# Kernel optimization log

Hardware: AMD Instinct MI355X
Metric: run time of the kernel (lower is better)

Reference implementation:

```python
import jax, jax.numpy as jnp
import numpy as np

B, T, C = 2, 2048, 2048
H, DK, DV, K = 16, 128, 128, 4
KEY_DIM = H * DK
VALUE_DIM = H * DV
CONV_DIM = 2 * KEY_DIM + VALUE_DIM
EPS = 1e-6


def setup_inputs() -> dict:
    key = jax.random.key(0)
    ks = jax.random.split(key, 6)
    s = 0.02
    return {
        "x": jax.random.normal(ks[0], (B, T, C), jnp.float32),
        "input_pos": jnp.arange(T, dtype=jnp.int32),
        "W_qkvz": jax.random.normal(ks[1], (C, CONV_DIM + VALUE_DIM), jnp.float32) * s,
        "W_b": jax.random.normal(ks[2], (C, H), jnp.float32) * s,
        "W_a": jax.random.normal(ks[3], (C, H), jnp.float32) * s,
        "conv_w": jax.random.normal(ks[4], (CONV_DIM, 1, K), jnp.float32) * 0.3,
        "norm_w": jnp.ones((DV,), jnp.float32),
        "W_out": jax.random.normal(ks[5], (VALUE_DIM, C), jnp.float32) * s,
        "conv_state": jnp.zeros((B, CONV_DIM, K), jnp.float32),
        "recurrent_state": jnp.zeros((B, H, DK, DV), jnp.float32),
    }


def _l2norm(a):
    return a / jnp.maximum(jnp.linalg.norm(a, axis=-1, keepdims=True), 1e-12)


def reference(x, input_pos, W_qkvz, W_b, W_a, conv_w, norm_w, W_out,
              conv_state, recurrent_state):
    Bx, Tx, Cx = x.shape
    # reset state when sequence starts at position 0
    keep = 1.0 - (input_pos[0] == 0).astype(x.dtype)
    conv_state = conv_state * keep
    recurrent_state = recurrent_state * keep

    qkvz = x @ W_qkvz                                  # [B,T,conv_dim+value_dim]
    qkv, z = qkvz[..., :CONV_DIM], qkvz[..., CONV_DIM:]
    z = z.reshape(Bx, Tx, H, DV)
    beta = jax.nn.sigmoid(x @ W_b)                     # [B,T,H]
    alpha = jax.nn.sigmoid(x @ W_a)                    # [B,T,H]

    # depthwise causal conv with carried conv_state prefix
    conv_in = jnp.concatenate([conv_state, qkv.transpose(0, 2, 1)], axis=-1)  # [B,conv_dim,K+T]
    y = jax.lax.conv_general_dilated(
        conv_in, conv_w, window_strides=(1,), padding='VALID',
        dimension_numbers=('NCH', 'OIH', 'NCH'), feature_group_count=CONV_DIM)
    y = jax.nn.silu(y[:, :, -Tx:]).transpose(0, 2, 1)  # [B,T,conv_dim]

    q, k, v = jnp.split(y, [KEY_DIM, 2 * KEY_DIM], axis=-1)
    q = _l2norm(q.reshape(Bx, Tx, H, DK))
    k = _l2norm(k.reshape(Bx, Tx, H, DK))
    v = v.reshape(Bx, Tx, H, DV)

    def step(state, xs):
        q_i, k_i, v_i, a_i, b_i = xs                    # [B,H,Dk],[B,H,Dk],[B,H,Dv],[B,H],[B,H]
        new_state = (a_i[..., None, None] * state
                     + b_i[..., None, None] * (k_i[..., :, None] * v_i[..., None, :]))
        out_i = jnp.einsum('bhk,bhkv->bhv', q_i, new_state)
        return new_state, out_i

    xs = (q.transpose(1, 0, 2, 3), k.transpose(1, 0, 2, 3), v.transpose(1, 0, 2, 3),
          alpha.transpose(1, 0, 2), beta.transpose(1, 0, 2))
    _, outs = jax.lax.scan(step, recurrent_state, xs)   # outs: [T,B,H,Dv]
    output = outs.transpose(1, 0, 2, 3)                 # [B,T,H,Dv]

    # RMSNorm over head_v_dim, then gate by sigmoid(z)
    output = output * jax.lax.rsqrt(jnp.mean(output * output, axis=-1, keepdims=True) + EPS) * norm_w
    output = output * jax.nn.sigmoid(z)
    return output.reshape(Bx, Tx, -1) @ W_out
```

## Files before the change

kernel.cpp:

```cpp
#include <hip/hip_runtime.h>
#include <hip/hip_bf16.h>
#include <math.h>

#define Bb 2
#define Tt 2048
#define Cc 2048
#define Hh 16
#define CONVD 6144
#define Mrows 4096
#define NCHUNK 32

typedef __attribute__((ext_vector_type(8))) short short8v;
typedef __attribute__((ext_vector_type(4))) float floatx4;

__device__ __forceinline__ unsigned short f2bf(float f) {
    __hip_bfloat16 h = __float2bfloat16(f);
    return __builtin_bit_cast(unsigned short, h);
}

__device__ __forceinline__ void load_lds16(const void* g, void* l) {
    __builtin_amdgcn_global_load_lds(
        (const __attribute__((address_space(1))) void*)g,
        (__attribute__((address_space(3))) void*)l, 16, 0, 0);
}

__device__ __forceinline__ int swz8(int col) {
    return col ^ (((col >> 5) & 3) << 3);
}

__global__ __launch_bounds__(256) void cast_bf16(
    const float* __restrict__ in, unsigned short* __restrict__ out, long n)
{
    long i = ((long)blockIdx.x * 256 + threadIdx.x) * 4;
    if (i + 3 >= n) return;
    float4 f = *(const float4*)(in + i);
    ushort4 o;
    o.x = f2bf(f.x); o.y = f2bf(f.y); o.z = f2bf(f.z); o.w = f2bf(f.w);
    *(ushort4*)(out + i) = o;
}

__global__ __launch_bounds__(256) void transpose_cast(
    const float* __restrict__ W, unsigned short* __restrict__ WT, int Kk, int Nn)
{
    __shared__ float tile[32][33];
    const int n0 = blockIdx.x * 32;
    const int k0 = blockIdx.y * 32;
    const int tx = threadIdx.x & 31;
    const int ty = threadIdx.x >> 5;
#pragma unroll
    for (int r = ty; r < 32; r += 8)
        tile[r][tx] = W[(size_t)(k0 + r) * Nn + n0 + tx];
    __syncthreads();
#pragma unroll
    for (int r = ty; r < 32; r += 8)
        WT[(size_t)(n0 + r) * Kk + k0 + tx] = f2bf(tile[tx][r]);
}

__global__ __launch_bounds__(256) void gemm_bf16(
    const unsigned short* __restrict__ A, const unsigned short* __restrict__ Bt,
    float* __restrict__ C, int Kk, int lda, int ldb, int ldc)
{
    __shared__ __align__(16) unsigned short A_lds[128 * 64];
    __shared__ __align__(16) unsigned short B_lds[128 * 64];

    const int tid = threadIdx.x;
    const int wv = tid >> 6;
    const int lane = tid & 63;
    const int wr = wv >> 1, wc = wv & 1;
    const int l15 = lane & 15, kq = lane >> 4;
    const int rsw = (l15 & 7) << 3;
    const int block_m = blockIdx.y * 128;
    const int block_n = blockIdx.x * 128;

    const int srow = lane >> 3;
    const int scol = ((lane & 7) ^ srow) << 3;

    floatx4 acc[4][4] = {};

    for (int k0 = 0; k0 < Kk; k0 += 64) {
#pragma unroll
        for (int i = 0; i < 4; ++i) {
            const int lq = wv * 4 + i;
            const unsigned short* asrc =
                A + (size_t)(block_m + lq * 8 + srow) * lda + k0 + scol;
            load_lds16(asrc, &A_lds[lq * 512]);
            const unsigned short* bsrc =
                Bt + (size_t)(block_n + lq * 8 + srow) * ldb + k0 + scol;
            load_lds16(bsrc, &B_lds[lq * 512]);
        }
        __syncthreads();

#pragma unroll
        for (int kk = 0; kk < 2; ++kk) {
            short8v af[4], bf[4];
#pragma unroll
            for (int mf = 0; mf < 4; ++mf) {
                const int row = wr * 64 + mf * 16 + l15;
                af[mf] = *(const short8v*)&A_lds[row * 64 + ((kk * 32 + kq * 8) ^ rsw)];
            }
#pragma unroll
            for (int nf = 0; nf < 4; ++nf) {
                const int row = wc * 64 + nf * 16 + l15;
                bf[nf] = *(const short8v*)&B_lds[row * 64 + ((kk * 32 + kq * 8) ^ rsw)];
            }
#pragma unroll
            for (int mf = 0; mf < 4; ++mf)
#pragma unroll
                for (int nf = 0; nf < 4; ++nf)
                    acc[mf][nf] = __builtin_amdgcn_mfma_f32_16x16x32_bf16(
                        af[mf], bf[nf], acc[mf][nf], 0, 0, 0);
        }
        __syncthreads();
    }

#pragma unroll
    for (int mf = 0; mf < 4; ++mf)
#pragma unroll
        for (int nf = 0; nf < 4; ++nf)
#pragma unroll
            for (int r = 0; r < 4; ++r) {
                int row = block_m + wr * 64 + mf * 16 + kq * 4 + r;
                int col = block_n + wc * 64 + nf * 16 + l15;
                C[(size_t)row * ldc + col] = acc[mf][nf][r];
            }
}

__global__ __launch_bounds__(256) void ab_kernel(
    const float* __restrict__ x, const float* __restrict__ W_b,
    const float* __restrict__ W_a, float* __restrict__ beta,
    float* __restrict__ alpha)
{
    const int row = blockIdx.x;
    const int tid = threadIdx.x;
    float acc[32];
#pragma unroll
    for (int u = 0; u < 32; ++u) acc[u] = 0.f;

    for (int k = tid; k < Cc; k += 256) {
        float xv = x[(size_t)row * Cc + k];
        const float4* wb = (const float4*)(W_b + (size_t)k * 16);
        const float4* wa = (const float4*)(W_a + (size_t)k * 16);
#pragma unroll
        for (int u = 0; u < 4; ++u) {
            float4 b4 = wb[u];
            float4 a4 = wa[u];
            acc[u * 4 + 0] = fmaf(xv, b4.x, acc[u * 4 + 0]);
            acc[u * 4 + 1] = fmaf(xv, b4.y, acc[u * 4 + 1]);
            acc[u * 4 + 2] = fmaf(xv, b4.z, acc[u * 4 + 2]);
            acc[u * 4 + 3] = fmaf(xv, b4.w, acc[u * 4 + 3]);
            acc[16 + u * 4 + 0] = fmaf(xv, a4.x, acc[16 + u * 4 + 0]);
            acc[16 + u * 4 + 1] = fmaf(xv, a4.y, acc[16 + u * 4 + 1]);
            acc[16 + u * 4 + 2] = fmaf(xv, a4.z, acc[16 + u * 4 + 2]);
            acc[16 + u * 4 + 3] = fmaf(xv, a4.w, acc[16 + u * 4 + 3]);
        }
    }
#pragma unroll
    for (int u = 0; u < 32; ++u) {
        float v = acc[u];
        for (int off = 32; off > 0; off >>= 1) v += __shfl_down(v, off);
        acc[u] = v;
    }
    __shared__ float red[4][32];
    const int wv = tid >> 6;
    if ((tid & 63) == 0) {
#pragma unroll
        for (int u = 0; u < 32; ++u) red[wv][u] = acc[u];
    }
    __syncthreads();
    if (tid < 32) {
        float v = red[0][tid] + red[1][tid] + red[2][tid] + red[3][tid];
        float s = 1.f / (1.f + expf(-v));
        if (tid < 16) beta[(size_t)row * 16 + tid] = s;
        else          alpha[(size_t)row * 16 + (tid - 16)] = s;
    }
}

__global__ __launch_bounds__(128) void conv_kernel(
    const float* __restrict__ qkv, const float* __restrict__ conv_w,
    const float* __restrict__ conv_state, const int* __restrict__ input_pos,
    float* __restrict__ qn, float* __restrict__ kn, float* __restrict__ vv)
{
    const int tc = blockIdx.x;
    const int hs = blockIdx.y;
    const int b  = blockIdx.z;
    const int lane = threadIdx.x;
    const int kind = hs >> 4;
    const int h = hs & 15;
    const int c = kind * 2048 + h * 128 + lane;
    const int t0 = tc * 8;
    const float keep = (input_pos[0] == 0) ? 0.f : 1.f;

    const float4 w4 = *(const float4*)(conv_w + (size_t)c * 4);

    float win0, win1, win2;
    {
        float tmp[3];
#pragma unroll
        for (int j = 0; j < 3; ++j) {
            int tau = t0 - 3 + j;
            tmp[j] = (tau >= 0) ? qkv[(size_t)(b * Tt + tau) * CONVD + c]
                   : keep * conv_state[((size_t)b * CONVD + c) * 4 + (tau + 4)];
        }
        win0 = tmp[0]; win1 = tmp[1]; win2 = tmp[2];
    }

    float y[8];
    __shared__ float red[8][2];
#pragma unroll
    for (int i = 0; i < 8; ++i) {
        float xv = qkv[(size_t)(b * Tt + t0 + i) * CONVD + c];
        float a = fmaf(w4.x, win0, fmaf(w4.y, win1, fmaf(w4.z, win2, w4.w * xv)));
        float yy = a / (1.f + expf(-a));
        win0 = win1; win1 = win2; win2 = xv;
        if (kind == 2) {
            vv[(size_t)(b * Tt + t0 + i) * 2048 + h * 128 + lane] = yy;
        } else {
            float sq = yy * yy;
            for (int off = 32; off > 0; off >>= 1) sq += __shfl_down(sq, off);
            if ((lane & 63) == 0) red[i][lane >> 6] = sq;
            y[i] = yy;
        }
    }
    if (kind == 2) return;
    __syncthreads();
#pragma unroll
    for (int i = 0; i < 8; ++i) {
        float tot = red[i][0] + red[i][1];
        float inv = 1.f / fmaxf(sqrtf(tot), 1e-12f);
        float outv = y[i] * inv;
        const size_t oidx = (size_t)(b * Tt + t0 + i) * 2048 + h * 128 + lane;
        if (kind == 0) qn[oidx] = outv;
        else           kn[oidx] = outv;
    }
}

__global__ __launch_bounds__(256) void chunk_prep(
    const float* __restrict__ kn, const float* __restrict__ vv,
    const float* __restrict__ alpha, const float* __restrict__ beta,
    float* __restrict__ logc_g, float* __restrict__ Mbuf)
{
    const int c = blockIdx.x, h = blockIdx.y, b = blockIdx.z;
    const int tid = threadIdx.x;
    const size_t bh = (size_t)b * Hh + h;

    __shared__ float K_lds[32][128];
    __shared__ float V_lds[32][128];
    __shared__ float logc_lds[64];
    __shared__ float b_lds[64];
    __shared__ float wk_lds[64];

    if (tid < 64) {
        const int row = b * Tt + c * 64 + tid;
        float a = alpha[(size_t)row * 16 + h];
        float la = logf(a);
#pragma unroll
        for (int d = 1; d < 64; d <<= 1) {
            float n = __shfl_up(la, d);
            if (tid >= d) la += n;
        }
        logc_lds[tid] = la;
        logc_g[bh * Tt + c * 64 + tid] = la;
        b_lds[tid] = beta[(size_t)row * 16 + h];
    }
    __syncthreads();
    if (tid < 64) {
        wk_lds[tid] = expf(logc_lds[63] - logc_lds[tid]) * b_lds[tid];
    }
    __syncthreads();

    const int ti = tid >> 4;
    const int tj = tid & 15;
    const int tj8sw = swz8(tj * 8);
    float acc[8][8];
#pragma unroll
    for (int i = 0; i < 8; ++i)
#pragma unroll
        for (int j = 0; j < 8; ++j) acc[i][j] = 0.f;

    for (int half = 0; half < 2; ++half) {
        {
            const int sl = tid >> 3;
            const int c0 = (tid & 7) * 16;
            const int grow = b * Tt + c * 64 + half * 32 + sl;
            const float4* kp = (const float4*)(kn + (size_t)grow * 2048 + h * 128 + c0);
            const float4* vp = (const float4*)(vv + (size_t)grow * 2048 + h * 128 + c0);
#pragma unroll
            for (int u = 0; u < 4; ++u) {
                const int cl = c0 + u * 4;
                *(float4*)(&K_lds[sl][cl]) = kp[u];
                *(float4*)(&V_lds[sl][swz8(cl)]) = vp[u];
            }
        }
        __syncthreads();
#pragma unroll 4
        for (int s = 0; s < 32; ++s) {
            float w = wk_lds[half * 32 + s];
            float4 k0 = *(const float4*)(&K_lds[s][ti * 8]);
            float4 k1 = *(const float4*)(&K_lds[s][ti * 8 + 4]);
            float4 v0 = *(const float4*)(&V_lds[s][tj8sw]);
            float4 v1 = *(const float4*)(&V_lds[s][tj8sw + 4]);
            float wk[8] = {w*k0.x, w*k0.y, w*k0.z, w*k0.w, w*k1.x, w*k1.y, w*k1.z, w*k1.w};
            float vf[8] = {v0.x, v0.y, v0.z, v0.w, v1.x, v1.y, v1.z, v1.w};
#pragma unroll
            for (int i = 0; i < 8; ++i)
#pragma unroll
                for (int j = 0; j < 8; ++j)
                    acc[i][j] = fmaf(wk[i], vf[j], acc[i][j]);
        }
        __syncthreads();
    }
    float* mb = Mbuf + ((bh * NCHUNK) + c) * 16384;
#pragma unroll
    for (int i = 0; i < 8; ++i) {
        float4 o0 = {acc[i][0], acc[i][1], acc[i][2], acc[i][3]};
        float4 o1 = {acc[i][4], acc[i][5], acc[i][6], acc[i][7]};
        *(float4*)(mb + (size_t)(ti * 8 + i) * 128 + tj * 8) = o0;
        *(float4*)(mb + (size_t)(ti * 8 + i) * 128 + tj * 8 + 4) = o1;
    }
}

__global__ __launch_bounds__(256) void state_scan(
    float* __restrict__ Mbuf, const float* __restrict__ logc_g,
    const float* __restrict__ rec_state, const int* __restrict__ input_pos)
{
    const size_t g = (size_t)blockIdx.x * 256 + threadIdx.x;
    const int bh = (int)(g >> 14);
    const float keep = (input_pos[0] == 0) ? 0.f : 1.f;

    float S = keep * rec_state[g];
    const float* lc = logc_g + (size_t)bh * Tt;
    float* base = Mbuf + (size_t)(g & ~16383ull) * NCHUNK + (g & 16383);
#pragma unroll 4
    for (int c = 0; c < NCHUNK; ++c) {
        float Atot = expf(lc[c * 64 + 63]);
        float m = base[(size_t)c * 16384];
        base[(size_t)c * 16384] = S;
        S = fmaf(Atot, S, m);
    }
}

__global__ __launch_bounds__(256) void chunk_out(
    const float* __restrict__ qn, const float* __restrict__ kn,
    const float* __restrict__ vv, const float* __restrict__ beta,
    const float* __restrict__ logc_g, const float* __restrict__ Sstates,
    const float* __restrict__ norm_w, const float* __restrict__ zbuf,
    unsigned short* __restrict__ gated_b)
{
    const int c = blockIdx.x, h = blockIdx.y, b = blockIdx.z;
    const int tid = threadIdx.x;
    const int ti = tid >> 4;
    const int tj = tid & 15;
    const size_t bh = (size_t)b * Hh + h;
    const int row0 = b * Tt + c * 64;

    __shared__ float Q_lds[64][132];
    __shared__ float Bf[64 * 68];
    __shared__ float At[64][68];
    __shared__ float logc_s[64], b_s[64];

    {
        const int r = tid >> 2, c0 = (tid & 3) * 32;
        const float4* qp = (const float4*)(qn + (size_t)(row0 + r) * 2048 + h * 128 + c0);
#pragma unroll
        for (int u = 0; u < 8; ++u)
            *(float4*)(&Q_lds[r][c0 + u * 4]) = qp[u];
    }
    if (tid < 64) {
        logc_s[tid] = logc_g[bh * Tt + c * 64 + tid];
        b_s[tid] = beta[(size_t)(row0 + tid) * 16 + h];
    }

    float acc_a[4][4] = {};
    for (int kh = 0; kh < 2; ++kh) {
        __syncthreads();
        {
            const int s = tid >> 2, c0 = (tid & 3) * 16;
            const float* kp = kn + (size_t)(row0 + s) * 2048 + h * 128 + kh * 64 + c0;
#pragma unroll
            for (int u = 0; u < 16; ++u)
                Bf[(c0 + u) * 68 + s] = kp[u];
        }
        __syncthreads();
#pragma unroll 4
        for (int kk = 0; kk < 64; ++kk) {
            float a[4];
#pragma unroll
            for (int r = 0; r < 4; ++r) a[r] = Q_lds[ti * 4 + r][kh * 64 + kk];
            float4 bq = *(const float4*)(&Bf[kk * 68 + tj * 4]);
            float bb[4] = {bq.x, bq.y, bq.z, bq.w};
#pragma unroll
            for (int r = 0; r < 4; ++r)
#pragma unroll
                for (int cc = 0; cc < 4; ++cc)
                    acc_a[r][cc] = fmaf(a[r], bb[cc], acc_a[r][cc]);
        }
    }

#pragma unroll
    for (int r = 0; r < 4; ++r) {
        const int t = ti * 4 + r;
        const float lct = logc_s[t];
#pragma unroll
        for (int cc = 0; cc < 4; ++cc) {
            const int s = tj * 4 + cc;
            float w = (s <= t) ? expf(lct - logc_s[s]) * b_s[s] : 0.f;
            At[t][s] = w * acc_a[r][cc];
        }
    }

    float o[4][8] = {};
    const float* Sbase = Sstates + (bh * NCHUNK + c) * 16384;
    const int tj8sw = swz8(tj * 8);
    for (int kb = 0; kb < 8; ++kb) {
        __syncthreads();
        {
            const int rr = tid >> 4;
            const int cl = (tid & 15) * 8;
            const int sw = swz8(cl);
            const float4* sp = (const float4*)(Sbase + (size_t)(kb * 16 + rr) * 128 + cl);
            *(float4*)(&Bf[rr * 132 + sw]) = sp[0];
            *(float4*)(&Bf[rr * 132 + sw + 4]) = sp[1];
        }
        __syncthreads();
#pragma unroll
        for (int kk = 0; kk < 16; ++kk) {
            float a[4];
#pragma unroll
            for (int r = 0; r < 4; ++r) a[r] = Q_lds[ti * 4 + r][kb * 16 + kk];
            float4 s0 = *(const float4*)(&Bf[kk * 132 + tj8sw]);
            float4 s1 = *(const float4*)(&Bf[kk * 132 + tj8sw + 4]);
            float sv[8] = {s0.x, s0.y, s0.z, s0.w, s1.x, s1.y, s1.z, s1.w};
#pragma unroll
            for (int r = 0; r < 4; ++r)
#pragma unroll
                for (int j = 0; j < 8; ++j)
                    o[r][j] = fmaf(a[r], sv[j], o[r][j]);
        }
    }
#pragma unroll
    for (int r = 0; r < 4; ++r) {
        const float ct = expf(logc_s[ti * 4 + r]);
#pragma unroll
        for (int j = 0; j < 8; ++j) o[r][j] *= ct;
    }

    for (int sh = 0; sh < 2; ++sh) {
        __syncthreads();
        {
            const int rr = tid >> 3;
            const int c0 = (tid & 7) * 16;
            const float4* vp = (const float4*)(vv + (size_t)(row0 + sh * 32 + rr) * 2048 + h * 128 + c0);
#pragma unroll
            for (int u = 0; u < 4; ++u) {
                const int cl = c0 + u * 4;
                *(float4*)(&Bf[rr * 132 + swz8(cl)]) = vp[u];
            }
        }
        __syncthreads();
#pragma unroll 2
        for (int sp = 0; sp < 32; ++sp) {
            const int s = sh * 32 + sp;
            float a[4];
#pragma unroll
            for (int r = 0; r < 4; ++r) a[r] = At[ti * 4 + r][s];
            float4 v0 = *(const float4*)(&Bf[sp * 132 + tj8sw]);
            float4 v1 = *(const float4*)(&Bf[sp * 132 + tj8sw + 4]);
            float vf[8] = {v0.x, v0.y, v0.z, v0.w, v1.x, v1.y, v1.z, v1.w};
#pragma unroll
            for (int r = 0; r < 4; ++r)
#pragma unroll
                for (int j = 0; j < 8; ++j)
                    o[r][j] = fmaf(a[r], vf[j], o[r][j]);
        }
    }

#pragma unroll
    for (int r = 0; r < 4; ++r) {
        float ss = 0.f;
#pragma unroll
        for (int j = 0; j < 8; ++j) ss = fmaf(o[r][j], o[r][j], ss);
        ss += __shfl_xor(ss, 1);
        ss += __shfl_xor(ss, 2);
        ss += __shfl_xor(ss, 4);
        ss += __shfl_xor(ss, 8);
        const float scale = rsqrtf(ss * (1.f / 128.f) + 1e-6f);
        const int t = ti * 4 + r;
        const float* zp = zbuf + (size_t)(row0 + t) * 2048 + h * 128 + tj * 8;
        unsigned short* gp = gated_b + (size_t)(row0 + t) * 2048 + h * 128 + tj * 8;
#pragma unroll
        for (int j = 0; j < 8; ++j) {
            float zv = zp[j];
            float g = o[r][j] * scale * norm_w[tj * 8 + j] * (1.f / (1.f + expf(-zv)));
            gp[j] = f2bf(g);
        }
    }
}

extern "C" void kernel_launch(void* const* d_in, const int* in_sizes, int n_in,
                              void* d_out, int out_size, void* d_ws, size_t ws_size,
                              hipStream_t stream) {
    (void)in_sizes; (void)n_in; (void)out_size; (void)ws_size;
    const float* x          = (const float*)d_in[0];
    const int*   input_pos  = (const int*)d_in[1];
    const float* W_qkvz     = (const float*)d_in[2];
    const float* W_b        = (const float*)d_in[3];
    const float* W_a        = (const float*)d_in[4];
    const float* conv_w     = (const float*)d_in[5];
    const float* norm_w     = (const float*)d_in[6];
    const float* W_out      = (const float*)d_in[7];
    const float* conv_state = (const float*)d_in[8];
    const float* rec_state  = (const float*)d_in[9];
    float* out = (float*)d_out;
    float* ws  = (float*)d_ws;

    float* qkv   = ws;
    float* Mbuf  = ws;
    unsigned short* gated_b = (unsigned short*)(ws + 16777216);
    float* qn    = ws + 25165824ull;
    float* kn    = qn + 8388608ull;
    float* vv    = kn + 8388608ull;
    unsigned short* xb  = (unsigned short*)qn;
    unsigned short* WqT = (unsigned short*)(qn + 4194304ull);
    float* zbuf  = vv + 8388608ull;
    unsigned short* WoT = (unsigned short*)(zbuf + 8388608ull);
    float* alpha = zbuf + 8388608ull + 2097152ull;
    float* beta  = alpha + 65536ull;
    float* logc  = beta + 65536ull;

    cast_bf16<<<8192, 256, 0, stream>>>(x, xb, 8388608L);
    transpose_cast<<<dim3(8192 / 32, 2048 / 32), 256, 0, stream>>>(W_qkvz, WqT, 2048, 8192);
    transpose_cast<<<dim3(2048 / 32, 2048 / 32), 256, 0, stream>>>(W_out, WoT, 2048, 2048);

    gemm_bf16<<<dim3(CONVD / 128, Mrows / 128), 256, 0, stream>>>(
        xb, WqT, qkv, 2048, 2048, 2048, CONVD);
    gemm_bf16<<<dim3(2048 / 128, Mrows / 128), 256, 0, stream>>>(
        xb, WqT + 6144ull * 2048, zbuf, 2048, 2048, 2048, 2048);
    ab_kernel<<<Mrows, 256, 0, stream>>>(x, W_b, W_a, beta, alpha);
    conv_kernel<<<dim3(Tt / 8, 48, Bb), 128, 0, stream>>>(
        qkv, conv_w, conv_state, input_pos, qn, kn, vv);
    chunk_prep<<<dim3(NCHUNK, Hh, Bb), 256, 0, stream>>>(
        kn, vv, alpha, beta, logc, Mbuf);
    state_scan<<<2048, 256, 0, stream>>>(Mbuf, logc, rec_state, input_pos);
    chunk_out<<<dim3(NCHUNK, Hh, Bb), 256, 0, stream>>>(
        qn, kn, vv, beta, logc, Mbuf, norm_w, zbuf, gated_b);
    gemm_bf16<<<dim3(2048 / 128, Mrows / 128), 256, 0, stream>>>(
        gated_b, WoT, out, 2048, 2048, 2048, 2048);
}
```

Measured before the change: 576.1 us.

## Merge QKV and Z projections into one 256x256-tile double-buffered bf16 GEMM

Replaces the two 128x128-tile GEMM launches for the qkv and z projections with a single 512-thread kernel. It uses 256x256 output tiles, double-buffered LDS filled by direct global-to-LDS loads, explicit waitcnt and barrier scheduling, and block-index swizzling. Each output tile is routed to either the qkv or z buffer by its column range. The goal is more operand reuse per LDS load, overlap of the next K-slice load with the MFMAs, and one less launch. The cost is heavy register use (128 accumulator floats per thread) and a grid of only 512 blocks.

```diff
diff --git a/kernel.cpp b/kernel.cpp
--- a/kernel.cpp
+++ b/kernel.cpp
@@ -28,6 +28,12 @@
     return col ^ (((col >> 5) & 3) << 3);
 }
 
+#define LGKM0 asm volatile("s_waitcnt lgkmcnt(0)" ::: "memory")
+#define VMC4  asm volatile("s_waitcnt vmcnt(4)" ::: "memory")
+#define VMC0  asm volatile("s_waitcnt vmcnt(0)" ::: "memory")
+#define SCHB  __builtin_amdgcn_sched_barrier(0)
+#define SBAR  __builtin_amdgcn_s_barrier()
+
 __global__ __launch_bounds__(256) void cast_bf16(
     const float* __restrict__ in, unsigned short* __restrict__ out, long n)
 {
@@ -54,6 +60,96 @@
 #pragma unroll
     for (int r = ty; r < 32; r += 8)
         WT[(size_t)(n0 + r) * Kk + k0 + tx] = f2bf(tile[tx][r]);
+}
+
+__global__ __launch_bounds__(512) void gemm256(
+    const unsigned short* __restrict__ A, const unsigned short* __restrict__ Bt,
+    float* __restrict__ C1, float* __restrict__ C2,
+    int Kk, int lda, int ldb)
+{
+    __shared__ __align__(16) unsigned short A_lds[2][256 * 32];
+    __shared__ __align__(16) unsigned short B_lds[2][256 * 32];
+
+    const int tid  = threadIdx.x;
+    const int wid  = tid >> 6;
+    const int lane = tid & 63;
+    const int wr = wid >> 2, wc = wid & 3;
+    const int l15 = lane & 15, kq = lane >> 4;
+    const int rdsw = (kq ^ ((l15 >> 1) & 3)) * 8;
+    const int rr = lane >> 2;
+    const int ch = (lane & 3) ^ ((lane >> 3) & 3);
+
+    const int nwg = gridDim.x * gridDim.y;
+    int bid = blockIdx.y * gridDim.x + blockIdx.x;
+    int swz = (bid & 7) * (nwg >> 3) + (bid >> 3);
+    const int block_m = (swz / gridDim.x) * 256;
+    const int block_n = (swz % gridDim.x) * 256;
+
+    const int NT = Kk >> 5;
+
+#define STAGE256(t) do {                                                     \
+    const int kk0 = (t) << 5;                                                \
+    unsigned short* la = &A_lds[(t) & 1][0];                                 \
+    unsigned short* lb = &B_lds[(t) & 1][0];                                 \
+    _Pragma("unroll")                                                        \
+    for (int i_ = 0; i_ < 2; ++i_) {                                         \
+        const int g_ = wid * 2 + i_;                                         \
+        load_lds16(A + (size_t)(block_m + g_ * 16 + rr) * lda + kk0 + ch * 8,\
+                   la + g_ * 512);                                           \
+        load_lds16(Bt + (size_t)(block_n + g_ * 16 + rr) * ldb + kk0 + ch * 8,\
+                   lb + g_ * 512);                                           \
+    }                                                                        \
+} while (0)
+
+    floatx4 acc[8][4] = {};
+
+    STAGE256(0);
+    STAGE256(1);
+    VMC4; SCHB; SBAR; SCHB;
+
+    for (int t = 0; t < NT; ++t) {
+        const unsigned short* la = &A_lds[t & 1][0];
+        const unsigned short* lb = &B_lds[t & 1][0];
+        short8v af[8], bf[4];
+#pragma unroll
+        for (int mf = 0; mf < 8; ++mf)
+            af[mf] = *(const short8v*)(la + (wr * 128 + mf * 16 + l15) * 32 + rdsw);
+#pragma unroll
+        for (int nf = 0; nf < 4; ++nf)
+            bf[nf] = *(const short8v*)(lb + (wc * 64 + nf * 16 + l15) * 32 + rdsw);
+        LGKM0; SCHB;
+        SBAR;
+        SCHB;
+        if (t + 2 < NT) STAGE256(t + 2);
+        SCHB;
+        __builtin_amdgcn_s_setprio(1);
+#pragma unroll
+        for (int mf = 0; mf < 8; ++mf)
+#pragma unroll
+            for (int nf = 0; nf < 4; ++nf)
+                acc[mf][nf] = __builtin_amdgcn_mfma_f32_16x16x32_bf16(
+                    af[mf], bf[nf], acc[mf][nf], 0, 0, 0);
+        __builtin_amdgcn_s_setprio(0);
+        SCHB;
+        if (t + 2 < NT)      { VMC4; }
+        else if (t + 1 < NT) { VMC0; }
+        SCHB; SBAR; SCHB;
+    }
+
+    float* Cp; int col0; size_t ldc;
+    if (block_n < 6144) { Cp = C1; col0 = block_n;        ldc = 6144; }
+    else                { Cp = C2; col0 = block_n - 6144; ldc = 2048; }
+#pragma unroll
+    for (int mf = 0; mf < 8; ++mf)
+#pragma unroll
+        for (int nf = 0; nf < 4; ++nf)
+#pragma unroll
+            for (int r = 0; r < 4; ++r) {
+                int row = block_m + wr * 128 + mf * 16 + kq * 4 + r;
+                int col = col0 + wc * 64 + nf * 16 + l15;
+                Cp[(size_t)row * ldc + col] = acc[mf][nf][r];
+            }
+#undef STAGE256
 }
 
 __global__ __launch_bounds__(256) void gemm_bf16(
@@ -531,10 +627,8 @@
     transpose_cast<<<dim3(8192 / 32, 2048 / 32), 256, 0, stream>>>(W_qkvz, WqT, 2048, 8192);
     transpose_cast<<<dim3(2048 / 32, 2048 / 32), 256, 0, stream>>>(W_out, WoT, 2048, 2048);
 
-    gemm_bf16<<<dim3(CONVD / 128, Mrows / 128), 256, 0, stream>>>(
-        xb, WqT, qkv, 2048, 2048, 2048, CONVD);
-    gemm_bf16<<<dim3(2048 / 128, Mrows / 128), 256, 0, stream>>>(
-        xb, WqT + 6144ull * 2048, zbuf, 2048, 2048, 2048, 2048);
+    gemm256<<<dim3(8192 / 256, Mrows / 256), 512, 0, stream>>>(
+        xb, WqT, qkv, zbuf, 2048, 2048, 2048);
     ab_kernel<<<Mrows, 256, 0, stream>>>(x, W_b, W_a, beta, alpha);
     conv_kernel<<<dim3(Tt / 8, 48, Bb), 128, 0, stream>>>(
         qkv, conv_w, conv_state, input_pos, qn, kn, vv);
```

Measured after the change: 558.2 us. -3.1%, faster.
